# Kernel tuning notes

Hardware: AMD Instinct MI355X
Metric: run time of the kernel (lower is better)

Reference implementation:

```python
import jax, jax.numpy as jnp
import numpy as np

SCALE = 4.0  # InputEmbedding scale
D = 16       # coordinate dim (InputEmbedding input_dim)


def _p(k, shape, s=0.05):
    return jax.random.normal(k, shape, dtype=jnp.float32) * s


def setup_inputs() -> dict:
    key = jax.random.key(0)
    ks = jax.random.split(key, 20)
    T, N, E, H = 8, 2048, 256, 768
    return {
        "observed": jax.random.normal(ks[0], (T, N, D), dtype=jnp.float32),
        "emb_W": _p(ks[1], (E, D)), "emb_b": _p(ks[2], (E,)),
        "e1_Wih": _p(ks[3], (3 * H, E)), "e1_Whh": _p(ks[4], (3 * H, H)),
        "e1_bih": _p(ks[5], (3 * H,)), "e1_bhh": _p(ks[6], (3 * H,)),
        "e2_Wih": _p(ks[7], (3 * H, E + H)), "e2_Whh": _p(ks[8], (3 * H, H)),
        "e2_bih": _p(ks[9], (3 * H,)), "e2_bhh": _p(ks[10], (3 * H,)),
        "dec_Wih": _p(ks[11], (3 * H, E)), "dec_Whh": _p(ks[12], (3 * H, H)),
        "dec_bih": _p(ks[13], (3 * H,)), "dec_bhh": _p(ks[14], (3 * H,)),
        "h2n_W": _p(ks[15], (5, H)), "h2n_b": _p(ks[16], (5,)),
        "mix_W": _p(ks[17], (D, 5)), "mix_b": _p(ks[18], (D,)),
        "n_predict": 12,
    }


def _gru(x, h, Wih, Whh, bih, bhh):
    # torch.nn.GRUCell math
    gi = x @ Wih.T + bih          # [N, 3H]
    gh = h @ Whh.T + bhh          # [N, 3H]
    ir, iz, in_ = jnp.split(gi, 3, axis=-1)
    hr, hz, hn = jnp.split(gh, 3, axis=-1)
    r = jax.nn.sigmoid(ir + hr)
    z = jax.nn.sigmoid(iz + hz)
    n = jnp.tanh(in_ + r * hn)
    return (1.0 - z) * n + z * h


def reference(observed, emb_W, emb_b,
              e1_Wih, e1_Whh, e1_bih, e1_bhh,
              e2_Wih, e2_Whh, e2_bih, e2_bhh,
              dec_Wih, dec_Whh, dec_bih, dec_bhh,
              h2n_W, h2n_b, mix_W, mix_b, n_predict):
    T, N, _ = observed.shape
    H = e1_Whh.shape[1]
    embed = lambda v: (SCALE * v) @ emb_W.T + emb_b   # InputEmbedding
    h0 = jnp.zeros((N, H), observed.dtype)

    # --- backward (inverse-time) encoder1 pass ---
    inv = observed[::-1]
    vel_b = inv[:-1] - inv[1:]          # obs2 - obs1 on reversed sequence, [T-1, N, D]
    def step1(h, v):
        return _gru(embed(v), h, e1_Wih, e1_Whh, e1_bih, e1_bhh), None
    h_inv, _ = jax.lax.scan(step1, h0, vel_b)
    # NOTE: original mutates the python hidden_state list in place, so every
    # h_invs entry aliases the FINAL encoder1 state -> h_inv is constant over t.

    # --- forward encoder2 pass (input = [embed(vel), h_inv]) ---
    vel_f = observed[1:] - observed[:-1]   # [T-1, N, D]
    def step2(h, v):
        x = jnp.concatenate([embed(v), h_inv], axis=1)
        return _gru(x, h, e2_Wih, e2_Whh, e2_bih, e2_bhh), None
    h, _ = jax.lax.scan(step2, h0, vel_f)

    def h2n(hs):
        # Hidden2Normal: linear then constrain sigmas / correlation
        n = hs @ h2n_W.T + h2n_b
        return jnp.concatenate(
            [n[:, :2], 0.01 + 0.2 * jax.nn.softplus(n[:, 2:4]), 0.7 * jnp.tanh(n[:, 4:5])],
            axis=1)

    def dec_step(h, obs1, obs2):
        h = _gru(embed(obs2 - obs1), h, dec_Wih, dec_Whh, dec_bih, dec_bhh)
        normal = h2n(h)                                   # [N, 5]
        pos = obs2 + jax.nn.relu(normal @ mix_W.T + mix_b)  # mix: Linear(5 -> 16)
        return h, normal, pos

    # decoder step i=0: (observed[-2], observed[-1]); i=1: (observed[-1], positions[-1].detach())
    h, n0, p0 = dec_step(h, observed[-2], observed[-1])
    h, n1, p1 = dec_step(h, observed[-1], jax.lax.stop_gradient(p0))

    def scan_step(carry, _):
        h, pm2, pm1 = carry
        h, n, p = dec_step(h, jax.lax.stop_gradient(pm2), jax.lax.stop_gradient(pm1))
        return (h, pm1, p), (n, p)
    _, (ns, ps) = jax.lax.scan(scan_step, (h, p0, p1), None, length=n_predict - 2)

    rel_pred_scene = jnp.concatenate([jnp.stack([n0, n1]), ns], axis=0)  # [n_predict, N, 5]
    pred_scene = jnp.concatenate([jnp.stack([p0, p1]), ps], axis=0)      # [n_predict, N, 16]
    return rel_pred_scene, pred_scene
```

## Files before the change

### kernel.cpp

```cpp
#include <hip/hip_runtime.h>
#include <hip/hip_bf16.h>
#include <math.h>

#define H 768
#define NB 2048
#define DD 16

typedef __attribute__((ext_vector_type(8))) short bf16x8;
typedef __attribute__((ext_vector_type(4))) float f32x4;

__device__ __forceinline__ void gload_lds16(const void* g, void* lds) {
  __builtin_amdgcn_global_load_lds((const __attribute__((address_space(1))) void*)g,
                                   (__attribute__((address_space(3))) void*)lds, 16, 0, 0);
}
__device__ __forceinline__ float b2f(short s) {
  union { unsigned int u; float f; } c;
  c.u = ((unsigned int)(unsigned short)s) << 16;
  return c.f;
}
__device__ __forceinline__ short f2bs(float f) {
  __hip_bfloat16 h = __float2bfloat16(f);
  return *(short*)&h;
}

__global__ void k_m1(const float* __restrict__ e1W, const float* __restrict__ e2W,
                     const float* __restrict__ dW, const float* __restrict__ embW,
                     float* __restrict__ M1) {
  int idx = blockIdx.x * 256 + threadIdx.x;
  if (idx >= 3 * 2304 * 16) return;
  int d = idx & 15, g = (idx >> 4) % 2304, s = idx / (2304 * 16);
  const float* W = s == 0 ? e1W : s == 1 ? e2W : dW;
  int ld = s == 1 ? 1024 : 256;
  float sum = 0.f;
  for (int e = 0; e < 256; ++e) sum += W[(size_t)g * ld + e] * embW[e * 16 + d];
  M1[idx] = 4.0f * sum;
}

__global__ void k_biasP(const float* __restrict__ e1W, const float* __restrict__ e2W,
                        const float* __restrict__ dW, const float* __restrict__ embB,
                        const float* b1i, const float* b1h, const float* b2i, const float* b2h,
                        const float* b3i, const float* b3h, float* __restrict__ out) {
  int idx = blockIdx.x * 256 + threadIdx.x;
  if (idx >= 3 * 3072) return;
  int c = idx % 3072, s = idx / 3072;
  int f = (c >> 4) & 3, u = (c >> 6) * 16 + (c & 15);
  const float* W = s == 0 ? e1W : s == 1 ? e2W : dW;
  int ld = s == 1 ? 1024 : 256;
  const float* bi = s == 0 ? b1i : s == 1 ? b2i : b3i;
  const float* bh = s == 0 ? b1h : s == 1 ? b2h : b3h;
  float v;
  if (f == 3) {
    v = bh[1536 + u];
  } else {
    int g = (f < 2 ? f * 768 : 1536) + u;
    float acc = bi[g] + (f < 2 ? bh[g] : 0.f);
    for (int e = 0; e < 256; ++e) acc += W[(size_t)g * ld + e] * embB[e];
    v = acc;
  }
  out[idx] = v;
}

__global__ void k_packB(const float* __restrict__ Whh, const float* __restrict__ M1s,
                        __hip_bfloat16* __restrict__ Bp) {
  int idx = blockIdx.x * 256 + threadIdx.x;
  if (idx >= 3072 * 800) return;
  int k = idx % 800, c = idx / 800;
  int f = (c >> 4) & 3, u = (c >> 6) * 16 + (c & 15);
  float v = 0.f;
  if (k < 768) {
    if (f == 0) v = Whh[(size_t)u * 768 + k];
    else if (f == 1) v = Whh[(size_t)(768 + u) * 768 + k];
    else if (f == 3) v = Whh[(size_t)(1536 + u) * 768 + k];
  } else if (k < 784) {
    if (f < 3) v = M1s[(size_t)(f * 768 + u) * 16 + (k - 768)];
  }
  Bp[idx] = __float2bfloat16(v);
}

__global__ void k_packB2g(const float* __restrict__ e2W, __hip_bfloat16* __restrict__ B2g) {
  int idx = blockIdx.x * 256 + threadIdx.x;
  if (idx >= 3072 * 768) return;
  int k = idx % 768, c = idx / 768;
  int f = (c >> 4) & 3, u = (c >> 6) * 16 + (c & 15);
  float v = (f < 3) ? e2W[(size_t)(f * 768 + u) * 1024 + 256 + k] : 0.f;
  B2g[idx] = __float2bfloat16(v);
}

__global__ void k_vel(const float* __restrict__ obs, __hip_bfloat16* __restrict__ velall) {
  int idx = blockIdx.x * 256 + threadIdx.x;
  if (idx >= 7 * 2048 * 32) return;
  int d = idx & 31, n = (idx >> 5) & 2047, s = idx >> 16;
  float v = 0.f;
  if (d < 16)
    v = obs[((size_t)(s + 1) * NB + n) * DD + d] - obs[((size_t)s * NB + n) * DD + d];
  velall[idx] = __float2bfloat16(v);
}

__global__ __launch_bounds__(256) void k_plain(
    const __hip_bfloat16* __restrict__ A, const __hip_bfloat16* __restrict__ B,
    __hip_bfloat16* __restrict__ C, int ldc) {
  __shared__ __align__(16) __hip_bfloat16 Asm[128 * 32];
  __shared__ __align__(16) __hip_bfloat16 Bsm[128 * 32];
  const int tid = threadIdx.x;
  const int w = tid >> 6, l = tid & 63;
  const int bm = blockIdx.y, bn = blockIdx.x;
  const int wm = w >> 1, wn = w & 1;
  const int lr = l & 15, lk = l >> 4;
  f32x4 acc[4][4];
#pragma unroll
  for (int m = 0; m < 4; ++m)
#pragma unroll
    for (int n = 0; n < 4; ++n) acc[m][n] = (f32x4){0.f, 0.f, 0.f, 0.f};
  const int rowA = bm * 128, rowB = bn * 128;
  const int off0 = w * 1024 + l * 16;
  for (int kb = 0; kb < H; kb += 32) {
#pragma unroll
    for (int i = 0; i < 2; ++i) {
      int o = i * 4096 + off0;
      int r = o >> 6, kk = (o & 63) >> 1;
      gload_lds16(A + (size_t)(rowA + r) * H + kb + kk, (char*)Asm + i * 4096 + w * 1024);
      gload_lds16(B + (size_t)(rowB + r) * H + kb + kk, (char*)Bsm + i * 4096 + w * 1024);
    }
    __syncthreads();
    bf16x8 af[4], bfr[4];
#pragma unroll
    for (int m = 0; m < 4; ++m)
      af[m] = *(const bf16x8*)(Asm + (wm * 64 + m * 16 + lr) * 32 + lk * 8);
#pragma unroll
    for (int n = 0; n < 4; ++n)
      bfr[n] = *(const bf16x8*)(Bsm + (wn * 64 + n * 16 + lr) * 32 + lk * 8);
#pragma unroll
    for (int m = 0; m < 4; ++m)
#pragma unroll
      for (int n = 0; n < 4; ++n)
        acc[m][n] = __builtin_amdgcn_mfma_f32_16x16x32_bf16(af[m], bfr[n], acc[m][n], 0, 0, 0);
    __syncthreads();
  }
#pragma unroll
  for (int m = 0; m < 4; ++m)
#pragma unroll
    for (int n = 0; n < 4; ++n) {
      int col = bn * 128 + wn * 64 + n * 16 + lr;
#pragma unroll
      for (int r4 = 0; r4 < 4; ++r4) {
        int row = rowA + wm * 64 + m * 16 + lk * 4 + r4;
        C[(size_t)row * ldc + col] = __float2bfloat16(acc[m][n][r4]);
      }
    }
}

__global__ __launch_bounds__(256) void k_step(
    const __hip_bfloat16* __restrict__ hin,
    const __hip_bfloat16* __restrict__ vel,
    const __hip_bfloat16* __restrict__ Bp,
    const float* __restrict__ bias,
    const __hip_bfloat16* __restrict__ g2a,
    __hip_bfloat16* __restrict__ hout) {
  __shared__ __align__(16) char lds[36864];
  const int tid = threadIdx.x;
  const int w = tid >> 6, l = tid & 63;
  const int nt = blockIdx.x, bm = blockIdx.y;
  const int rowA = bm * 128, colB = nt * 64;
  const int lr = l & 15, lk = l >> 4;
  const int wbase = w * 1024;
  const int ce = (tid & 3) * 8, rA = tid >> 2;

  auto STAGE = [&](int bufo, int kb) {
#pragma unroll
    for (int i_ = 0; i_ < 2; ++i_) {
      int r_ = i_ * 64 + rA;
      const __hip_bfloat16* s_ = (kb < 768)
          ? hin + (size_t)(rowA + r_) * H + kb + ce
          : vel + (size_t)(rowA + r_) * 32 + ce;
      gload_lds16(s_, lds + bufo + i_ * 4096 + wbase);
    }
    gload_lds16(Bp + (size_t)(colB + rA) * 800 + kb + ce, lds + bufo + 8192 + wbase);
  };

  f32x4 acc[2][4];
#pragma unroll
  for (int m = 0; m < 2; ++m)
#pragma unroll
    for (int n = 0; n < 4; ++n) acc[m][n] = (f32x4){0.f, 0.f, 0.f, 0.f};

  const int bo[3] = {0, 12288, 24576};
  STAGE(bo[0], 0);
  STAGE(bo[1], 32);

  for (int ki = 0; ki < 25; ++ki) {
    if (ki < 24) asm volatile("s_waitcnt vmcnt(3)" ::: "memory");
    else         asm volatile("s_waitcnt vmcnt(0)" ::: "memory");
    __builtin_amdgcn_sched_barrier(0);
    __builtin_amdgcn_s_barrier();
    __builtin_amdgcn_sched_barrier(0);
    if (ki < 23) STAGE(bo[(ki + 2) % 3], (ki + 2) * 32);
    const int cur = bo[ki % 3];
    const __hip_bfloat16* Ab = (const __hip_bfloat16*)(lds + cur);
    const __hip_bfloat16* Bb = (const __hip_bfloat16*)(lds + cur + 8192);
    bf16x8 a0 = *(const bf16x8*)(Ab + (w * 32 + lr) * 32 + lk * 8);
    bf16x8 a1 = *(const bf16x8*)(Ab + (w * 32 + 16 + lr) * 32 + lk * 8);
    bf16x8 b0 = *(const bf16x8*)(Bb + lr * 32 + lk * 8);
    bf16x8 b1 = *(const bf16x8*)(Bb + (16 + lr) * 32 + lk * 8);
    const bool last = (ki == 24);
    bf16x8 b2 = *(const bf16x8*)(Bb + ((last ? 32 : 48) + lr) * 32 + lk * 8);
    acc[0][0] = __builtin_amdgcn_mfma_f32_16x16x32_bf16(a0, b0, acc[0][0], 0, 0, 0);
    acc[1][0] = __builtin_amdgcn_mfma_f32_16x16x32_bf16(a1, b0, acc[1][0], 0, 0, 0);
    acc[0][1] = __builtin_amdgcn_mfma_f32_16x16x32_bf16(a0, b1, acc[0][1], 0, 0, 0);
    acc[1][1] = __builtin_amdgcn_mfma_f32_16x16x32_bf16(a1, b1, acc[1][1], 0, 0, 0);
    if (last) {
      acc[0][2] = __builtin_amdgcn_mfma_f32_16x16x32_bf16(a0, b2, acc[0][2], 0, 0, 0);
      acc[1][2] = __builtin_amdgcn_mfma_f32_16x16x32_bf16(a1, b2, acc[1][2], 0, 0, 0);
    } else {
      acc[0][3] = __builtin_amdgcn_mfma_f32_16x16x32_bf16(a0, b2, acc[0][3], 0, 0, 0);
      acc[1][3] = __builtin_amdgcn_mfma_f32_16x16x32_bf16(a1, b2, acc[1][3], 0, 0, 0);
    }
  }

  __syncthreads();
  short* T = (short*)lds;
  const float* bp = bias + nt * 64;
#pragma unroll
  for (int n = 0; n < 4; ++n) {
    float bv = bp[n * 16 + lr];
#pragma unroll
    for (int m = 0; m < 2; ++m) {
      int rbase = w * 32 + m * 16 + lk * 4;
#pragma unroll
      for (int r4 = 0; r4 < 4; ++r4)
        T[(rbase + r4) * 72 + n * 16 + lr] = f2bs(acc[m][n][r4] + bv);
    }
  }
  __syncthreads();

  const int row = tid >> 1;
  const int ub = (tid & 1) * 8;
  const size_t grow = (size_t)(rowA + row);
  const short* Tp = T + row * 72;
  bf16x8 Lr = *(const bf16x8*)(Tp + ub);
  bf16x8 Lz = *(const bf16x8*)(Tp + 16 + ub);
  bf16x8 Li = *(const bf16x8*)(Tp + 32 + ub);
  bf16x8 Lh = *(const bf16x8*)(Tp + 48 + ub);
  bf16x8 h8 = *(const bf16x8*)(hin + grow * H + nt * 16 + ub);
  bf16x8 gr, gz, gi_;
  if (g2a) {
    const __hip_bfloat16* gp = g2a + grow * 3072 + nt * 64;
    gr  = *(const bf16x8*)(gp + ub);
    gz  = *(const bf16x8*)(gp + 16 + ub);
    gi_ = *(const bf16x8*)(gp + 32 + ub);
  }
  union { bf16x8 v; short s[8]; } ob;
#pragma unroll
  for (int e = 0; e < 8; ++e) {
    float xr = b2f(Lr[e]), xz = b2f(Lz[e]), xi = b2f(Li[e]), xh = b2f(Lh[e]);
    if (g2a) { xr += b2f(gr[e]); xz += b2f(gz[e]); xi += b2f(gi_[e]); }
    float r = 1.f / (1.f + expf(-xr));
    float z = 1.f / (1.f + expf(-xz));
    float nn = tanhf(xi + r * xh);
    float hv = (1.f - z) * nn + z * b2f(h8[e]);
    ob.s[e] = f2bs(hv);
  }
  *(bf16x8*)(hout + grow * H + nt * 16 + ub) = ob.v;
}

__global__ void k_head(const __hip_bfloat16* __restrict__ h, const float* __restrict__ obs2,
                       const float* __restrict__ h2n_W, const float* __restrict__ h2n_b,
                       const float* __restrict__ mix_W, const float* __restrict__ mix_b,
                       float* __restrict__ rel_out, float* __restrict__ pos_out,
                       __hip_bfloat16* __restrict__ velout) {
  int wv = threadIdx.x >> 6, lane = threadIdx.x & 63;
  int row = blockIdx.x * 4 + wv;
  float s0 = 0.f, s1 = 0.f, s2 = 0.f, s3 = 0.f, s4 = 0.f;
  for (int k = lane; k < H; k += 64) {
    float hv = b2f(((const short*)h)[(size_t)row * H + k]);
    s0 += hv * h2n_W[k];
    s1 += hv * h2n_W[H + k];
    s2 += hv * h2n_W[2 * H + k];
    s3 += hv * h2n_W[3 * H + k];
    s4 += hv * h2n_W[4 * H + k];
  }
#pragma unroll
  for (int off = 32; off; off >>= 1) {
    s0 += __shfl_down(s0, off);
    s1 += __shfl_down(s1, off);
    s2 += __shfl_down(s2, off);
    s3 += __shfl_down(s3, off);
    s4 += __shfl_down(s4, off);
  }
  s0 = __shfl(s0, 0); s1 = __shfl(s1, 0); s2 = __shfl(s2, 0);
  s3 = __shfl(s3, 0); s4 = __shfl(s4, 0);
  float n0 = s0 + h2n_b[0], n1 = s1 + h2n_b[1];
  float x2 = s2 + h2n_b[2], x3 = s3 + h2n_b[3], x4 = s4 + h2n_b[4];
  float n2 = 0.01f + 0.2f * (x2 > 0.f ? x2 + log1pf(expf(-x2)) : log1pf(expf(x2)));
  float n3 = 0.01f + 0.2f * (x3 > 0.f ? x3 + log1pf(expf(-x3)) : log1pf(expf(x3)));
  float n4 = 0.7f * tanhf(x4);
  float rl = 0.f;
  if (lane < DD) {
    float a = mix_b[lane] + n0 * mix_W[lane * 5 + 0] + n1 * mix_W[lane * 5 + 1] +
              n2 * mix_W[lane * 5 + 2] + n3 * mix_W[lane * 5 + 3] + n4 * mix_W[lane * 5 + 4];
    rl = a > 0.f ? a : 0.f;
    pos_out[(size_t)row * DD + lane] = obs2[(size_t)row * DD + lane] + rl;
  }
  if (lane < 32)
    velout[(size_t)row * 32 + lane] = __float2bfloat16(lane < DD ? rl : 0.f);
  if (lane == 0) {
    rel_out[(size_t)row * 5 + 0] = n0;
    rel_out[(size_t)row * 5 + 1] = n1;
    rel_out[(size_t)row * 5 + 2] = n2;
    rel_out[(size_t)row * 5 + 3] = n3;
    rel_out[(size_t)row * 5 + 4] = n4;
  }
}

extern "C" void kernel_launch(void* const* d_in, const int* in_sizes, int n_in,
                              void* d_out, int out_size, void* d_ws, size_t ws_size,
                              hipStream_t stream) {
  (void)in_sizes; (void)n_in; (void)out_size; (void)ws_size;
  const float* observed = (const float*)d_in[0];
  const float* emb_W   = (const float*)d_in[1];
  const float* emb_b   = (const float*)d_in[2];
  const float* e1_Wih  = (const float*)d_in[3];
  const float* e1_Whh  = (const float*)d_in[4];
  const float* e1_bih  = (const float*)d_in[5];
  const float* e1_bhh  = (const float*)d_in[6];
  const float* e2_Wih  = (const float*)d_in[7];
  const float* e2_Whh  = (const float*)d_in[8];
  const float* e2_bih  = (const float*)d_in[9];
  const float* e2_bhh  = (const float*)d_in[10];
  const float* dec_Wih = (const float*)d_in[11];
  const float* dec_Whh = (const float*)d_in[12];
  const float* dec_bih = (const float*)d_in[13];
  const float* dec_bhh = (const float*)d_in[14];
  const float* h2n_W   = (const float*)d_in[15];
  const float* h2n_b   = (const float*)d_in[16];
  const float* mix_W   = (const float*)d_in[17];
  const float* mix_b   = (const float*)d_in[18];

  char* p = (char*)d_ws;
  auto alloc = [&](size_t bytes) { char* r = p; p += (bytes + 255) & ~(size_t)255; return r; };

  __hip_bfloat16* hz     = (__hip_bfloat16*)alloc((size_t)NB * H * 2);
  __hip_bfloat16* hp0    = (__hip_bfloat16*)alloc((size_t)NB * H * 2);
  __hip_bfloat16* hp1    = (__hip_bfloat16*)alloc((size_t)NB * H * 2);
  __hip_bfloat16* velall = (__hip_bfloat16*)alloc((size_t)7 * NB * 32 * 2);
  __hip_bfloat16* dvel   = (__hip_bfloat16*)alloc((size_t)NB * 32 * 2);
  __hip_bfloat16* Bp1    = (__hip_bfloat16*)alloc((size_t)3072 * 800 * 2);
  __hip_bfloat16* Bp2    = (__hip_bfloat16*)alloc((size_t)3072 * 800 * 2);
  __hip_bfloat16* Bp3    = (__hip_bfloat16*)alloc((size_t)3072 * 800 * 2);
  __hip_bfloat16* B2g    = (__hip_bfloat16*)alloc((size_t)3072 * 768 * 2);
  __hip_bfloat16* g2add  = (__hip_bfloat16*)alloc((size_t)NB * 3072 * 2);
  float*          M1     = (float*)alloc((size_t)3 * 2304 * 16 * 4);
  float*          biasP  = (float*)alloc((size_t)3 * 3072 * 4);

  hipMemsetAsync(hz, 0, (size_t)NB * H * 2, stream);
  k_m1<<<(3 * 2304 * 16 + 255) / 256, 256, 0, stream>>>(e1_Wih, e2_Wih, dec_Wih, emb_W, M1);
  k_biasP<<<(3 * 3072 + 255) / 256, 256, 0, stream>>>(e1_Wih, e2_Wih, dec_Wih, emb_b,
                                                      e1_bih, e1_bhh, e2_bih, e2_bhh,
                                                      dec_bih, dec_bhh, biasP);
  k_packB<<<(3072 * 800 + 255) / 256, 256, 0, stream>>>(e1_Whh, M1, Bp1);
  k_packB<<<(3072 * 800 + 255) / 256, 256, 0, stream>>>(e2_Whh, M1 + 2304 * 16, Bp2);
  k_packB<<<(3072 * 800 + 255) / 256, 256, 0, stream>>>(dec_Whh, M1 + 2 * 2304 * 16, Bp3);
  k_packB2g<<<(3072 * 768 + 255) / 256, 256, 0, stream>>>(e2_Wih, B2g);
  k_vel<<<(7 * NB * 32 + 255) / 256, 256, 0, stream>>>(observed, velall);

  dim3 gs(48, 16);
  const __hip_bfloat16* src;
  __hip_bfloat16* dst = hp0;

  src = hz;
  for (int t = 0; t < 7; ++t) {
    k_step<<<gs, 256, 0, stream>>>(src, velall + (size_t)(6 - t) * NB * 32, Bp1, biasP,
                                   nullptr, dst);
    src = dst;
    dst = (dst == hp0) ? hp1 : hp0;
  }
  k_plain<<<dim3(24, 16), 256, 0, stream>>>(src, B2g, g2add, 3072);

  src = hz;
  for (int t = 0; t < 7; ++t) {
    k_step<<<gs, 256, 0, stream>>>(src, velall + (size_t)t * NB * 32, Bp2, biasP + 3072,
                                   g2add, dst);
    src = dst;
    dst = (dst == hp0) ? hp1 : hp0;
  }

  float* rel  = (float*)d_out;
  float* pred = (float*)d_out + (size_t)12 * NB * 5;
  for (int k = 0; k < 12; ++k) {
    const __hip_bfloat16* vk = (k == 0) ? velall + (size_t)6 * NB * 32 : dvel;
    k_step<<<gs, 256, 0, stream>>>(src, vk, Bp3, biasP + 2 * 3072, nullptr, dst);
    const float* o2 = (k == 0) ? observed + (size_t)7 * NB * DD
                               : pred + (size_t)(k - 1) * NB * DD;
    k_head<<<NB / 4, 256, 0, stream>>>(dst, o2, h2n_W, h2n_b, mix_W, mix_b,
                                       rel + (size_t)k * NB * 5, pred + (size_t)k * NB * DD,
                                       dvel);
    src = dst;
    dst = (dst == hp0) ? hp1 : hp0;
  }
}
```

Measured before the change: 865.1 us.

## Swizzle LDS layout, deepen step pipeline to 4 stages, merge packB launches

Applies an XOR swizzle to the k-offset of LDS tiles in both the plain GEMM and the recurrent step kernel, to reduce bank conflicts on MFMA fragment reads. The step kernel goes from a 3-buffer to a 4-buffer prefetch pipeline, with matching vmcnt waits, a fully unrolled k loop, and s_setprio raised around the MFMA block. The three packB launches are merged into a single launch with a 2D grid. The extra LDS (48KB) may lower occupancy, and the swizzle has to match exactly between the global-to-LDS writes and the fragment reads.

```diff
diff --git a/kernel.cpp b/kernel.cpp
--- a/kernel.cpp
+++ b/kernel.cpp
@@ -60,10 +60,16 @@
   out[idx] = v;
 }
 
-__global__ void k_packB(const float* __restrict__ Whh, const float* __restrict__ M1s,
-                        __hip_bfloat16* __restrict__ Bp) {
+__global__ void k_packB3(const float* __restrict__ W1, const float* __restrict__ W2,
+                         const float* __restrict__ W3, const float* __restrict__ M1all,
+                         __hip_bfloat16* __restrict__ B1, __hip_bfloat16* __restrict__ B2,
+                         __hip_bfloat16* __restrict__ B3) {
   int idx = blockIdx.x * 256 + threadIdx.x;
   if (idx >= 3072 * 800) return;
+  int s = blockIdx.y;
+  const float* Whh = s == 0 ? W1 : s == 1 ? W2 : W3;
+  const float* M1s = M1all + (size_t)s * 2304 * 16;
+  __hip_bfloat16* Bp = s == 0 ? B1 : s == 1 ? B2 : B3;
   int k = idx % 800, c = idx / 800;
   int f = (c >> 4) & 3, u = (c >> 6) * 16 + (c & 15);
   float v = 0.f;
@@ -106,29 +112,30 @@
   const int bm = blockIdx.y, bn = blockIdx.x;
   const int wm = w >> 1, wn = w & 1;
   const int lr = l & 15, lk = l >> 4;
+  const int ks = (((tid & 3) ^ ((tid >> 3) & 3)) << 3);
+  const int lks = ((lk ^ ((lr >> 1) & 3)) << 3);
   f32x4 acc[4][4];
 #pragma unroll
   for (int m = 0; m < 4; ++m)
 #pragma unroll
     for (int n = 0; n < 4; ++n) acc[m][n] = (f32x4){0.f, 0.f, 0.f, 0.f};
   const int rowA = bm * 128, rowB = bn * 128;
-  const int off0 = w * 1024 + l * 16;
+  const int rA = tid >> 2;
   for (int kb = 0; kb < H; kb += 32) {
 #pragma unroll
     for (int i = 0; i < 2; ++i) {
-      int o = i * 4096 + off0;
-      int r = o >> 6, kk = (o & 63) >> 1;
-      gload_lds16(A + (size_t)(rowA + r) * H + kb + kk, (char*)Asm + i * 4096 + w * 1024);
-      gload_lds16(B + (size_t)(rowB + r) * H + kb + kk, (char*)Bsm + i * 4096 + w * 1024);
+      int r = i * 64 + rA;
+      gload_lds16(A + (size_t)(rowA + r) * H + kb + ks, (char*)Asm + i * 4096 + w * 1024);
+      gload_lds16(B + (size_t)(rowB + r) * H + kb + ks, (char*)Bsm + i * 4096 + w * 1024);
     }
     __syncthreads();
     bf16x8 af[4], bfr[4];
 #pragma unroll
     for (int m = 0; m < 4; ++m)
-      af[m] = *(const bf16x8*)(Asm + (wm * 64 + m * 16 + lr) * 32 + lk * 8);
+      af[m] = *(const bf16x8*)(Asm + (wm * 64 + m * 16 + lr) * 32 + lks);
 #pragma unroll
     for (int n = 0; n < 4; ++n)
-      bfr[n] = *(const bf16x8*)(Bsm + (wn * 64 + n * 16 + lr) * 32 + lk * 8);
+      bfr[n] = *(const bf16x8*)(Bsm + (wn * 64 + n * 16 + lr) * 32 + lks);
 #pragma unroll
     for (int m = 0; m < 4; ++m)
 #pragma unroll
@@ -156,25 +163,27 @@
     const float* __restrict__ bias,
     const __hip_bfloat16* __restrict__ g2a,
     __hip_bfloat16* __restrict__ hout) {
-  __shared__ __align__(16) char lds[36864];
+  __shared__ __align__(16) char lds[49152];
   const int tid = threadIdx.x;
   const int w = tid >> 6, l = tid & 63;
   const int nt = blockIdx.x, bm = blockIdx.y;
   const int rowA = bm * 128, colB = nt * 64;
   const int lr = l & 15, lk = l >> 4;
   const int wbase = w * 1024;
-  const int ce = (tid & 3) * 8, rA = tid >> 2;
-
-  auto STAGE = [&](int bufo, int kb) {
+  const int rA = tid >> 2;
+  const int ce = (((tid & 3) ^ ((tid >> 3) & 3)) << 3);
+  const int lks = ((lk ^ ((lr >> 1) & 3)) << 3);
+
+  auto STAGE = [&](int buf, int kb) {
 #pragma unroll
     for (int i_ = 0; i_ < 2; ++i_) {
       int r_ = i_ * 64 + rA;
       const __hip_bfloat16* s_ = (kb < 768)
           ? hin + (size_t)(rowA + r_) * H + kb + ce
           : vel + (size_t)(rowA + r_) * 32 + ce;
-      gload_lds16(s_, lds + bufo + i_ * 4096 + wbase);
+      gload_lds16(s_, lds + buf * 12288 + i_ * 4096 + wbase);
     }
-    gload_lds16(Bp + (size_t)(colB + rA) * 800 + kb + ce, lds + bufo + 8192 + wbase);
+    gload_lds16(Bp + (size_t)(colB + rA) * 800 + kb + ce, lds + buf * 12288 + 8192 + wbase);
   };
 
   f32x4 acc[2][4];
@@ -183,26 +192,29 @@
 #pragma unroll
     for (int n = 0; n < 4; ++n) acc[m][n] = (f32x4){0.f, 0.f, 0.f, 0.f};
 
-  const int bo[3] = {0, 12288, 24576};
-  STAGE(bo[0], 0);
-  STAGE(bo[1], 32);
-
+  STAGE(0, 0);
+  STAGE(1, 32);
+  STAGE(2, 64);
+
+#pragma unroll
   for (int ki = 0; ki < 25; ++ki) {
-    if (ki < 24) asm volatile("s_waitcnt vmcnt(3)" ::: "memory");
-    else         asm volatile("s_waitcnt vmcnt(0)" ::: "memory");
+    if (ki < 23)      asm volatile("s_waitcnt vmcnt(6)" ::: "memory");
+    else if (ki == 23) asm volatile("s_waitcnt vmcnt(3)" ::: "memory");
+    else               asm volatile("s_waitcnt vmcnt(0)" ::: "memory");
     __builtin_amdgcn_sched_barrier(0);
     __builtin_amdgcn_s_barrier();
     __builtin_amdgcn_sched_barrier(0);
-    if (ki < 23) STAGE(bo[(ki + 2) % 3], (ki + 2) * 32);
-    const int cur = bo[ki % 3];
-    const __hip_bfloat16* Ab = (const __hip_bfloat16*)(lds + cur);
-    const __hip_bfloat16* Bb = (const __hip_bfloat16*)(lds + cur + 8192);
-    bf16x8 a0 = *(const bf16x8*)(Ab + (w * 32 + lr) * 32 + lk * 8);
-    bf16x8 a1 = *(const bf16x8*)(Ab + (w * 32 + 16 + lr) * 32 + lk * 8);
-    bf16x8 b0 = *(const bf16x8*)(Bb + lr * 32 + lk * 8);
-    bf16x8 b1 = *(const bf16x8*)(Bb + (16 + lr) * 32 + lk * 8);
+    if (ki < 22) STAGE((ki + 3) & 3, (ki + 3) * 32);
+    const char* cur = lds + (ki & 3) * 12288;
+    const __hip_bfloat16* Ab = (const __hip_bfloat16*)cur;
+    const __hip_bfloat16* Bb = (const __hip_bfloat16*)(cur + 8192);
+    bf16x8 a0 = *(const bf16x8*)(Ab + (w * 32 + lr) * 32 + lks);
+    bf16x8 a1 = *(const bf16x8*)(Ab + (w * 32 + 16 + lr) * 32 + lks);
+    bf16x8 b0 = *(const bf16x8*)(Bb + lr * 32 + lks);
+    bf16x8 b1 = *(const bf16x8*)(Bb + (16 + lr) * 32 + lks);
     const bool last = (ki == 24);
-    bf16x8 b2 = *(const bf16x8*)(Bb + ((last ? 32 : 48) + lr) * 32 + lk * 8);
+    bf16x8 b2 = *(const bf16x8*)(Bb + ((last ? 32 : 48) + lr) * 32 + lks);
+    __builtin_amdgcn_s_setprio(1);
     acc[0][0] = __builtin_amdgcn_mfma_f32_16x16x32_bf16(a0, b0, acc[0][0], 0, 0, 0);
     acc[1][0] = __builtin_amdgcn_mfma_f32_16x16x32_bf16(a1, b0, acc[1][0], 0, 0, 0);
     acc[0][1] = __builtin_amdgcn_mfma_f32_16x16x32_bf16(a0, b1, acc[0][1], 0, 0, 0);
@@ -214,6 +226,7 @@
       acc[0][3] = __builtin_amdgcn_mfma_f32_16x16x32_bf16(a0, b2, acc[0][3], 0, 0, 0);
       acc[1][3] = __builtin_amdgcn_mfma_f32_16x16x32_bf16(a1, b2, acc[1][3], 0, 0, 0);
     }
+    __builtin_amdgcn_s_setprio(0);
   }
 
   __syncthreads();
@@ -356,9 +369,8 @@
   k_biasP<<<(3 * 3072 + 255) / 256, 256, 0, stream>>>(e1_Wih, e2_Wih, dec_Wih, emb_b,
                                                       e1_bih, e1_bhh, e2_bih, e2_bhh,
                                                       dec_bih, dec_bhh, biasP);
-  k_packB<<<(3072 * 800 + 255) / 256, 256, 0, stream>>>(e1_Whh, M1, Bp1);
-  k_packB<<<(3072 * 800 + 255) / 256, 256, 0, stream>>>(e2_Whh, M1 + 2304 * 16, Bp2);
-  k_packB<<<(3072 * 800 + 255) / 256, 256, 0, stream>>>(dec_Whh, M1 + 2 * 2304 * 16, Bp3);
+  k_packB3<<<dim3((3072 * 800 + 255) / 256, 3), 256, 0, stream>>>(e1_Whh, e2_Whh, dec_Whh,
+                                                                  M1, Bp1, Bp2, Bp3);
   k_packB2g<<<(3072 * 768 + 255) / 256, 256, 0, stream>>>(e2_Wih, B2g);
   k_vel<<<(7 * NB * 32 + 255) / 256, 256, 0, stream>>>(observed, velall);
 
```

Result: faster. 773.3 us (-10.6%).
